# Optimization experiments

Measured on AMD Instinct MI355X. Metric: run time of the kernel, lower is better.

The kernel has to match this reference:

```python
import jax, jax.numpy as jnp
import numpy as np

DIM = 1024
NEXP = 8
TOPK = 2
B, S = 2, 2048
HID = 4 * DIM

# ---- BitLinear (kyegomez/BitNet, 1.58-bit) helpers ----

def rmsnorm(x):
    # SimpleRMSNorm: x / rms(x), no learned scale
    return x * jax.lax.rsqrt(jnp.mean(x * x, axis=-1, keepdims=True) + 1e-6)

def act_quant(x):
    # per-token int8 absmax quant
    scale = 127.0 / jnp.clip(jnp.max(jnp.abs(x), axis=-1, keepdims=True), 1e-5, None)
    return jnp.clip(jnp.round(x * scale), -128, 127) / scale

def weight_quant(w):
    # ternary weight quant with per-tensor mean-abs scale
    scale = 1.0 / jnp.clip(jnp.mean(jnp.abs(w)), 1e-5, None)
    return jnp.clip(jnp.round(w * scale), -1, 1) / scale

def ste(a, q):
    # straight-through estimator: forward q, backward identity on a
    return a + jax.lax.stop_gradient(q - a)

def bit_input(x):
    xn = rmsnorm(x)
    return ste(xn, act_quant(xn))

def bit_weight(w):
    return ste(w, weight_quant(w))


def setup_inputs() -> dict:
    key = jax.random.key(0)
    ks = jax.random.split(key, 6)
    x = jax.random.normal(ks[0], (B, S, DIM), dtype=jnp.float32)
    eps = jax.random.normal(ks[1], (B, S, NEXP), dtype=jnp.float32)
    w_route = jax.random.normal(ks[2], (NEXP, DIM), dtype=jnp.float32) * 0.02
    w_noise = jax.random.normal(ks[3], (NEXP, DIM), dtype=jnp.float32) * 0.02
    w1 = jax.random.normal(ks[4], (NEXP, HID, DIM), dtype=jnp.float32) * 0.02
    w2 = jax.random.normal(ks[5], (NEXP, DIM, HID), dtype=jnp.float32) * 0.02
    return {"x": x, "eps": eps, "w_route": w_route, "w_noise": w_noise, "w1": w1, "w2": w2}


def reference(x, eps, w_route, w_noise, w1, w2):
    Bb, Ss, D = x.shape
    # router: both BitLinears share the same rmsnorm+quant of x (no bias)
    xq = bit_input(x)                                  # [B,S,D]
    logits = xq @ bit_weight(w_route).T                # [B,S,E]
    noise_logits = xq @ bit_weight(w_noise).T          # [B,S,E]
    noisy = logits + eps * jax.nn.softplus(noise_logits)
    _, topi = jax.lax.top_k(noisy, TOPK)               # indices [B,S,K]
    sel = jnp.any(jax.nn.one_hot(topi, NEXP, dtype=jnp.bool_), axis=-2)  # [B,S,E]
    sparse = jnp.where(sel, noisy, -jnp.inf)
    gates = jax.nn.softmax(sparse, axis=-1)            # zeros at unselected experts

    T = Bb * Ss
    xf = xq.reshape(T, D)                              # expert layer-1 input quant == router's
    gf = gates.reshape(T, NEXP)
    w1q = jax.vmap(bit_weight)(w1)                     # [E,H,D]
    w2q = jax.vmap(bit_weight)(w2)                     # [E,D,H]
    h = jax.nn.relu(jnp.einsum('td,ehd->teh', xf, w1q))
    hq = bit_input(h)                                  # per-(token,expert) quant
    y = jnp.einsum('teh,edh->ted', hq, w2q)            # expert outputs
    # gated combine; gates are exactly 0 for unselected experts -> identical to masked scatter-add
    out = jnp.einsum('ted,te->td', y, gf)
    return out.reshape(Bb, Ss, D)
```

## Files before the change

### kernel.cpp

```cpp
#include <hip/hip_runtime.h>
#include <hip/hip_bf16.h>

#define DIMD 1024
#define NEXP 8
#define NTOK 4096
#define HIDN 4096
#define CAP  4096
#define EXPSTRIDE 4194304L

typedef __bf16 bf16;
typedef bf16  bf16x8 __attribute__((ext_vector_type(8)));
typedef bf16  bf16x4 __attribute__((ext_vector_type(4)));
typedef float f32x4  __attribute__((ext_vector_type(4)));

__device__ __forceinline__ void gload16(const void* g, void* l) {
  __builtin_amdgcn_global_load_lds(
      (const __attribute__((address_space(1))) unsigned int*)g,
      (__attribute__((address_space(3))) unsigned int*)l, 16, 0, 0);
}

#define VMCNT8 asm volatile("s_waitcnt vmcnt(8)" ::: "memory")
#define VMCNT0 asm volatile("s_waitcnt vmcnt(0)" ::: "memory")
#define BAR    __builtin_amdgcn_s_barrier()

__global__ void k_wsum(const float* __restrict__ w1, const float* __restrict__ w2,
                       float* __restrict__ partials) {
  const int slot = blockIdx.y;
  const int b = blockIdx.x;
  const int tid = threadIdx.x;
  const float* src = (slot < 8) ? (w1 + (long)slot * EXPSTRIDE)
                                : (w2 + (long)(slot - 8) * EXPSTRIDE);
  const f32x4* p = (const f32x4*)src;
  float s = 0.f;
  #pragma unroll
  for (int j = 0; j < 32; ++j) {
    f32x4 v = p[(long)b * 8192 + j * 256 + tid];
    s += fabsf(v.x) + fabsf(v.y) + fabsf(v.z) + fabsf(v.w);
  }
  #pragma unroll
  for (int o = 1; o < 64; o <<= 1) s += __shfl_xor(s, o, 64);
  __shared__ float red[4];
  if ((tid & 63) == 0) red[tid >> 6] = s;
  __syncthreads();
  if (tid == 0) partials[slot * 128 + b] = red[0] + red[1] + red[2] + red[3];
}

__global__ void k_finalize(const float* __restrict__ partials,
                           const float* __restrict__ wr, const float* __restrict__ wn,
                           float* __restrict__ wmean,
                           bf16* __restrict__ wrq, bf16* __restrict__ wnq) {
  const int tid = threadIdx.x;
  if (tid < 16) {
    float s = 0.f;
    for (int j = 0; j < 128; ++j) s += partials[tid * 128 + j];
    wmean[tid] = fmaxf(s * (1.0f / 4194304.0f), 1e-5f);
  }
  float sr = 0.f, sn = 0.f;
  #pragma unroll
  for (int j = 0; j < 32; ++j) {
    sr += fabsf(wr[j * 256 + tid]);
    sn += fabsf(wn[j * 256 + tid]);
  }
  #pragma unroll
  for (int o = 1; o < 64; o <<= 1) {
    sr += __shfl_xor(sr, o, 64);
    sn += __shfl_xor(sn, o, 64);
  }
  __shared__ float red[8];
  if ((tid & 63) == 0) { red[tid >> 6] = sr; red[4 + (tid >> 6)] = sn; }
  __syncthreads();
  if (tid == 0) {
    wmean[16] = fmaxf((red[0] + red[1] + red[2] + red[3]) * (1.0f / 8192.0f), 1e-5f);
    wmean[17] = fmaxf((red[4] + red[5] + red[6] + red[7]) * (1.0f / 8192.0f), 1e-5f);
  }
  __syncthreads();
  const float ir = 1.0f / wmean[16];
  const float in = 1.0f / wmean[17];
  for (int j = 0; j < 32; ++j) {
    int i = j * 256 + tid;
    wrq[i] = (bf16)fminf(fmaxf(rintf(wr[i] * ir), -1.f), 1.f);
    wnq[i] = (bf16)fminf(fmaxf(rintf(wn[i] * in), -1.f), 1.f);
  }
}

__global__ void k_wquant(const float* __restrict__ w1, const float* __restrict__ w2,
                         const float* __restrict__ wmean,
                         bf16* __restrict__ w1q, bf16* __restrict__ w2q) {
  const int tid = threadIdx.x;
  const int which = blockIdx.x >> 14;
  const long lg = (long)(blockIdx.x & 16383) * 256 + tid;
  const int e = (int)(lg >> 19);
  const float inv = 1.0f / wmean[(which ? 8 : 0) + e];
  const float* src = which ? w2 : w1;
  bf16* dst = which ? w2q : w1q;
  const f32x4* p = (const f32x4*)src + lg * 2;
  f32x4 v0 = p[0], v1 = p[1];
  bf16x8 q;
  q[0] = (bf16)fminf(fmaxf(rintf(v0.x * inv), -1.f), 1.f);
  q[1] = (bf16)fminf(fmaxf(rintf(v0.y * inv), -1.f), 1.f);
  q[2] = (bf16)fminf(fmaxf(rintf(v0.z * inv), -1.f), 1.f);
  q[3] = (bf16)fminf(fmaxf(rintf(v0.w * inv), -1.f), 1.f);
  q[4] = (bf16)fminf(fmaxf(rintf(v1.x * inv), -1.f), 1.f);
  q[5] = (bf16)fminf(fmaxf(rintf(v1.y * inv), -1.f), 1.f);
  q[6] = (bf16)fminf(fmaxf(rintf(v1.z * inv), -1.f), 1.f);
  q[7] = (bf16)fminf(fmaxf(rintf(v1.w * inv), -1.f), 1.f);
  *(bf16x8*)(dst + lg * 8) = q;
}

__global__ void k_xquant(const float* __restrict__ x, bf16* __restrict__ xq,
                         float* __restrict__ sx) {
  const int t = blockIdx.x, tid = threadIdx.x;
  f32x4 v = ((const f32x4*)(x + (long)t * DIMD))[tid];
  float ss = v.x * v.x + v.y * v.y + v.z * v.z + v.w * v.w;
  float am = fmaxf(fmaxf(fabsf(v.x), fabsf(v.y)), fmaxf(fabsf(v.z), fabsf(v.w)));
  #pragma unroll
  for (int o = 1; o < 64; o <<= 1) {
    ss += __shfl_xor(ss, o, 64);
    am = fmaxf(am, __shfl_xor(am, o, 64));
  }
  __shared__ float red[8];
  if ((tid & 63) == 0) { red[tid >> 6] = ss; red[4 + (tid >> 6)] = am; }
  __syncthreads();
  ss = red[0] + red[1] + red[2] + red[3];
  am = fmaxf(fmaxf(red[4], red[5]), fmaxf(red[6], red[7]));
  const float r = 1.0f / sqrtf(ss * (1.0f / DIMD) + 1e-6f);
  const float amn = fmaxf(am * r, 1e-5f);
  const float s = 127.0f / amn;
  bf16x4 q;
  q[0] = (bf16)fminf(fmaxf(rintf((v.x * r) * s), -128.f), 127.f);
  q[1] = (bf16)fminf(fmaxf(rintf((v.y * r) * s), -128.f), 127.f);
  q[2] = (bf16)fminf(fmaxf(rintf((v.z * r) * s), -128.f), 127.f);
  q[3] = (bf16)fminf(fmaxf(rintf((v.w * r) * s), -128.f), 127.f);
  *(bf16x4*)(xq + (long)t * DIMD + tid * 4) = q;
  if (tid == 0) sx[t] = amn * (1.0f / 127.0f);
}

__global__ void k_router(const bf16* __restrict__ xq, const float* __restrict__ sx,
                         const bf16* __restrict__ wrq, const bf16* __restrict__ wnq,
                         const float* __restrict__ eps, const float* __restrict__ wmean,
                         int* __restrict__ cnt, int* __restrict__ idx,
                         float* __restrict__ gate) {
  __shared__ float xf[DIMD];
  __shared__ float dots[16];
  const int t = blockIdx.x, tid = threadIdx.x;
  const bf16* xr = xq + (long)t * DIMD;
  #pragma unroll
  for (int j = 0; j < 4; ++j) xf[tid * 4 + j] = (float)xr[tid * 4 + j];
  __syncthreads();
  const int grp = tid >> 4, l16 = tid & 15;
  const bf16* wv = (grp < 8) ? (wrq + grp * DIMD) : (wnq + (grp - 8) * DIMD);
  float s = 0.f;
  #pragma unroll
  for (int j = 0; j < 64; ++j) s += xf[l16 + j * 16] * (float)wv[l16 + j * 16];
  s += __shfl_xor(s, 1, 64); s += __shfl_xor(s, 2, 64);
  s += __shfl_xor(s, 4, 64); s += __shfl_xor(s, 8, 64);
  if (l16 == 0) dots[grp] = s;
  __syncthreads();
  if (tid == 0) {
    const float st = sx[t];
    const float fr = st * wmean[16], fn = st * wmean[17];
    float ny[8];
    #pragma unroll
    for (int e = 0; e < 8; ++e) {
      const float nl = dots[8 + e] * fn;
      const float sp = fmaxf(nl, 0.f) + log1pf(expf(-fabsf(nl)));
      ny[e] = dots[e] * fr + eps[t * 8 + e] * sp;
    }
    int i1 = 0;
    #pragma unroll
    for (int e = 1; e < 8; ++e) if (ny[e] > ny[i1]) i1 = e;
    int i2 = (i1 == 0) ? 1 : 0;
    #pragma unroll
    for (int e = 0; e < 8; ++e) if (e != i1 && ny[e] > ny[i2]) i2 = e;
    const float ex = expf(ny[i2] - ny[i1]);
    const float g1 = 1.0f / (1.0f + ex);
    const float g2 = ex * g1;
    int p1 = atomicAdd(&cnt[i1], 1);
    idx[i1 * CAP + p1] = t; gate[i1 * CAP + p1] = g1;
    int p2 = atomicAdd(&cnt[i2], 1);
    idx[i2 * CAP + p2] = t; gate[i2 * CAP + p2] = g2;
  }
}

__global__ void k_offsets(const int* __restrict__ cnt, int* __restrict__ offs) {
  if (threadIdx.x == 0) {
    int a = 0;
    for (int e = 0; e < NEXP; ++e) { offs[e] = a; a += cnt[e]; }
    offs[8] = a;
  }
}

template <int KD, int LOGNT, bool L1>
__global__ __launch_bounds__(256, 2) void k_gemm(
    const bf16* __restrict__ Abase, const bf16* __restrict__ Wq,
    const int* __restrict__ cnt, const int* __restrict__ offs,
    const int* __restrict__ idx, const float* __restrict__ gate,
    const float* __restrict__ srow, const float* __restrict__ wmean,
    float* __restrict__ Out) {
  const int bid = blockIdx.x;
  const int xcd = bid & 7;
  const int s = bid >> 3;
  const int pl = s >> 5;
  const int mt = s & 31;
  const int pidx = pl * 8 + xcd;
  const int e = pidx >> LOGNT;
  const int nt = pidx & ((1 << LOGNT) - 1);

  const int c = cnt[e];
  if (mt * 128 >= c) return;
  const int oe = offs[e];
  __shared__ __align__(16) char lds[66048];
  char* lA0 = lds;
  char* lB0 = lds + 16384;
  char* lA1 = lds + 32768;
  char* lB1 = lds + 49152;
  int* tokL = (int*)(lds + 65536);
  const int tid = threadIdx.x, w = tid >> 6, lam = tid & 63;
  if (tid < 128) {
    int i = mt * 128 + tid;
    tokL[tid] = idx[e * CAP + (i < c ? i : c - 1)];
  }
  __syncthreads();

  const bf16* aP[4];
  const bf16* bP[4];
  #pragma unroll
  for (int i = 0; i < 4; ++i) {
    const int lrow = w * 32 + i * 8 + (lam >> 3);
    const int schunk = (lam & 7) ^ (lrow & 7);
    long arow;
    if (L1) arow = (long)tokL[lrow];
    else { int ii = mt * 128 + lrow; arow = (long)oe + (ii < c ? ii : c - 1); }
    aP[i] = Abase + arow * KD + schunk * 8;
    bP[i] = Wq + (long)e * EXPSTRIDE + (long)(nt * 128 + lrow) * KD + schunk * 8;
  }
  const int lbase = (w * 32) * 128 + lam * 16;

  auto STAGE = [&](int kb, char* dA, char* dB) {
    #pragma unroll
    for (int i = 0; i < 4; ++i) {
      gload16(aP[i] + kb * 64, dA + lbase + i * 1024);
      gload16(bP[i] + kb * 64, dB + lbase + i * 1024);
    }
  };

  const int wr = w >> 1, wc = w & 1;
  int offA[4][2], offB[4][2];
  #pragma unroll
  for (int m = 0; m < 4; ++m) {
    const int ra = wr * 64 + m * 16 + (lam & 15);
    const int rb = wc * 64 + m * 16 + (lam & 15);
    #pragma unroll
    for (int ks = 0; ks < 2; ++ks) {
      const int ch = ks * 4 + (lam >> 4);
      offA[m][ks] = ra * 128 + ((ch ^ (ra & 7)) << 4);
      offB[m][ks] = rb * 128 + ((ch ^ (rb & 7)) << 4);
    }
  }
  f32x4 acc[4][4];
  #pragma unroll
  for (int m = 0; m < 4; ++m)
    #pragma unroll
    for (int n = 0; n < 4; ++n) acc[m][n] = (f32x4){0.f, 0.f, 0.f, 0.f};

  auto COMPUTE = [&](const char* cA, const char* cB) {
    #pragma unroll
    for (int ks = 0; ks < 2; ++ks) {
      bf16x8 af[4], bfr[4];
      #pragma unroll
      for (int m = 0; m < 4; ++m) af[m] = *(const bf16x8*)(cA + offA[m][ks]);
      #pragma unroll
      for (int n = 0; n < 4; ++n) bfr[n] = *(const bf16x8*)(cB + offB[n][ks]);
      #pragma unroll
      for (int m = 0; m < 4; ++m)
        #pragma unroll
        for (int n = 0; n < 4; ++n)
          acc[m][n] = __builtin_amdgcn_mfma_f32_16x16x32_bf16(af[m], bfr[n], acc[m][n], 0, 0, 0);
    }
  };

  constexpr int KT = KD / 64;
  STAGE(0, lA0, lB0);
  for (int kb = 0; kb < KT; kb += 2) {
    STAGE(kb + 1, lA1, lB1);
    VMCNT8;
    BAR;
    COMPUTE(lA0, lB0);
    BAR;
    if (kb + 2 < KT) { STAGE(kb + 2, lA0, lB0); VMCNT8; } else { VMCNT0; }
    BAR;
    COMPUTE(lA1, lB1);
    BAR;
  }

  const float wm = wmean[(L1 ? 0 : 8) + e];
  #pragma unroll
  for (int m = 0; m < 4; ++m) {
    #pragma unroll
    for (int r = 0; r < 4; ++r) {
      const int rl = wr * 64 + m * 16 + ((lam >> 4) << 2) + r;
      const int i = mt * 128 + rl;
      if (i < c) {
        if (L1) {
          const float fac = srow[tokL[rl]] * wm;
          float* hp = Out + (long)(oe + i) * HIDN + nt * 128 + wc * 64 + (lam & 15);
          #pragma unroll
          for (int n = 0; n < 4; ++n) hp[n * 16] = fmaxf(acc[m][n][r] * fac, 0.f);
        } else {
          const float fac = srow[oe + i] * wm * gate[e * CAP + i];
          float* op = Out + (long)tokL[rl] * DIMD + nt * 128 + wc * 64 + (lam & 15);
          #pragma unroll
          for (int n = 0; n < 4; ++n) atomicAdd(op + n * 16, acc[m][n][r] * fac);
        }
      }
    }
  }
}

__global__ void k_hquant(const float* __restrict__ h, bf16* __restrict__ hq,
                         float* __restrict__ sh, const int* __restrict__ offs) {
  const int row = blockIdx.x;
  if (row >= offs[8]) return;
  const int tid = threadIdx.x;
  const f32x4* hr = (const f32x4*)(h + (long)row * HIDN);
  f32x4 v[4];
  float ss = 0.f, am = 0.f;
  #pragma unroll
  for (int j = 0; j < 4; ++j) {
    v[j] = hr[tid + j * 256];
    ss += v[j].x * v[j].x + v[j].y * v[j].y + v[j].z * v[j].z + v[j].w * v[j].w;
    am = fmaxf(am, fmaxf(fmaxf(fabsf(v[j].x), fabsf(v[j].y)),
                         fmaxf(fabsf(v[j].z), fabsf(v[j].w))));
  }
  #pragma unroll
  for (int o = 1; o < 64; o <<= 1) {
    ss += __shfl_xor(ss, o, 64);
    am = fmaxf(am, __shfl_xor(am, o, 64));
  }
  __shared__ float red[8];
  if ((tid & 63) == 0) { red[tid >> 6] = ss; red[4 + (tid >> 6)] = am; }
  __syncthreads();
  ss = red[0] + red[1] + red[2] + red[3];
  am = fmaxf(fmaxf(red[4], red[5]), fmaxf(red[6], red[7]));
  const float r = 1.0f / sqrtf(ss * (1.0f / HIDN) + 1e-6f);
  const float amn = fmaxf(am * r, 1e-5f);
  const float s = 127.0f / amn;
  bf16* dst = hq + (long)row * HIDN;
  #pragma unroll
  for (int j = 0; j < 4; ++j) {
    bf16x4 q;
    q[0] = (bf16)fminf(fmaxf(rintf((v[j].x * r) * s), -128.f), 127.f);
    q[1] = (bf16)fminf(fmaxf(rintf((v[j].y * r) * s), -128.f), 127.f);
    q[2] = (bf16)fminf(fmaxf(rintf((v[j].z * r) * s), -128.f), 127.f);
    q[3] = (bf16)fminf(fmaxf(rintf((v[j].w * r) * s), -128.f), 127.f);
    *(bf16x4*)(dst + (tid + j * 256) * 4) = q;
  }
  if (tid == 0) sh[row] = amn * (1.0f / 127.0f);
}

extern "C" void kernel_launch(void* const* d_in, const int* in_sizes, int n_in,
                              void* d_out, int out_size, void* d_ws, size_t ws_size,
                              hipStream_t stream) {
  const float* x   = (const float*)d_in[0];
  const float* eps = (const float*)d_in[1];
  const float* wr  = (const float*)d_in[2];
  const float* wn  = (const float*)d_in[3];
  const float* w1  = (const float*)d_in[4];
  const float* w2  = (const float*)d_in[5];
  float* out = (float*)d_out;
  (void)in_sizes; (void)n_in; (void)ws_size;

  char* ws = (char*)d_ws;
  size_t off = 0;
  auto alloc = [&](size_t bytes) -> void* {
    void* p = ws + off;
    off = (off + bytes + 255) & ~(size_t)255;
    return p;
  };
  bf16*  w1q      = (bf16*)alloc(67108864);
  bf16*  w2q      = (bf16*)alloc(67108864);
  bf16*  wrq      = (bf16*)alloc(16384);
  bf16*  wnq      = (bf16*)alloc(16384);
  bf16*  xq       = (bf16*)alloc(8388608);
  float* sx       = (float*)alloc(16384);
  float* sh       = (float*)alloc(32768);
  int*   idxb     = (int*)alloc(131072);
  float* gateb    = (float*)alloc(131072);
  int*   cntb     = (int*)alloc(64);
  int*   offsb    = (int*)alloc(64);
  float* partials = (float*)alloc(8192);
  float* wmean    = (float*)alloc(128);
  float* h        = (float*)alloc(134217728);
  bf16*  hq       = (bf16*)alloc(67108864);

  hipMemsetAsync(out, 0, (size_t)out_size * sizeof(float), stream);
  hipMemsetAsync(cntb, 0, 64, stream);

  k_wsum<<<dim3(128, 16), 256, 0, stream>>>(w1, w2, partials);
  k_finalize<<<1, 256, 0, stream>>>(partials, wr, wn, wmean, wrq, wnq);
  k_wquant<<<32768, 256, 0, stream>>>(w1, w2, wmean, w1q, w2q);
  k_xquant<<<NTOK, 256, 0, stream>>>(x, xq, sx);
  k_router<<<NTOK, 256, 0, stream>>>(xq, sx, wrq, wnq, eps, wmean, cntb, idxb, gateb);
  k_offsets<<<1, 64, 0, stream>>>(cntb, offsb);
  k_gemm<1024, 5, true><<<8192, 256, 0, stream>>>(
      xq, w1q, cntb, offsb, idxb, gateb, sx, wmean, h);
  k_hquant<<<8192, 256, 0, stream>>>(h, hq, sh, offsb);
  k_gemm<4096, 3, false><<<2048, 256, 0, stream>>>(
      hq, w2q, cntb, offsb, idxb, gateb, sh, wmean, out);
}
```

Before: 762.0 us.

## Switch expert GEMMs from bf16 to int8 MFMA with int8 quantized storage

Stores quantized weights, activations and hidden states as int8 instead of bf16, and replaces the bf16 16x16x32 MFMA with the i32 16x16x64 int8 MFMA. LDS staging, swizzle and load pointers are reworked for 64-byte int8 K tiles, which halves LDS use and lets launch bounds request 4 blocks per CU. Values are already integers within int8 range, so results should stay exact with int32 accumulation. This halves memory traffic for the quantized tensors and doubles MFMA throughput per instruction.

After: 661.3 us. 1.15x faster.

```diff
diff --git a/kernel.cpp b/kernel.cpp
--- a/kernel.cpp
+++ b/kernel.cpp
@@ -10,8 +10,11 @@
 
 typedef __bf16 bf16;
 typedef bf16  bf16x8 __attribute__((ext_vector_type(8)));
-typedef bf16  bf16x4 __attribute__((ext_vector_type(4)));
 typedef float f32x4  __attribute__((ext_vector_type(4)));
+typedef int   i32x4  __attribute__((ext_vector_type(4)));
+typedef signed char i8x8 __attribute__((ext_vector_type(8)));
+typedef signed char i8x4 __attribute__((ext_vector_type(4)));
+typedef signed char i8;
 
 __device__ __forceinline__ void gload16(const void* g, void* l) {
   __builtin_amdgcn_global_load_lds(
@@ -19,9 +22,9 @@
       (__attribute__((address_space(3))) unsigned int*)l, 16, 0, 0);
 }
 
-#define VMCNT8 asm volatile("s_waitcnt vmcnt(8)" ::: "memory")
+#define VMCNT4 asm volatile("s_waitcnt vmcnt(4)" ::: "memory")
 #define VMCNT0 asm volatile("s_waitcnt vmcnt(0)" ::: "memory")
-#define BAR    __builtin_amdgcn_s_barrier()
+#define BAR    asm volatile("s_barrier" ::: "memory")
 
 __global__ void k_wsum(const float* __restrict__ w1, const float* __restrict__ w2,
                        float* __restrict__ partials) {
@@ -85,29 +88,29 @@
 
 __global__ void k_wquant(const float* __restrict__ w1, const float* __restrict__ w2,
                          const float* __restrict__ wmean,
-                         bf16* __restrict__ w1q, bf16* __restrict__ w2q) {
+                         i8* __restrict__ w1q, i8* __restrict__ w2q) {
   const int tid = threadIdx.x;
   const int which = blockIdx.x >> 14;
   const long lg = (long)(blockIdx.x & 16383) * 256 + tid;
   const int e = (int)(lg >> 19);
   const float inv = 1.0f / wmean[(which ? 8 : 0) + e];
   const float* src = which ? w2 : w1;
-  bf16* dst = which ? w2q : w1q;
+  i8* dst = which ? w2q : w1q;
   const f32x4* p = (const f32x4*)src + lg * 2;
   f32x4 v0 = p[0], v1 = p[1];
-  bf16x8 q;
-  q[0] = (bf16)fminf(fmaxf(rintf(v0.x * inv), -1.f), 1.f);
-  q[1] = (bf16)fminf(fmaxf(rintf(v0.y * inv), -1.f), 1.f);
-  q[2] = (bf16)fminf(fmaxf(rintf(v0.z * inv), -1.f), 1.f);
-  q[3] = (bf16)fminf(fmaxf(rintf(v0.w * inv), -1.f), 1.f);
-  q[4] = (bf16)fminf(fmaxf(rintf(v1.x * inv), -1.f), 1.f);
-  q[5] = (bf16)fminf(fmaxf(rintf(v1.y * inv), -1.f), 1.f);
-  q[6] = (bf16)fminf(fmaxf(rintf(v1.z * inv), -1.f), 1.f);
-  q[7] = (bf16)fminf(fmaxf(rintf(v1.w * inv), -1.f), 1.f);
-  *(bf16x8*)(dst + lg * 8) = q;
-}
-
-__global__ void k_xquant(const float* __restrict__ x, bf16* __restrict__ xq,
+  i8x8 q;
+  q[0] = (i8)fminf(fmaxf(rintf(v0.x * inv), -1.f), 1.f);
+  q[1] = (i8)fminf(fmaxf(rintf(v0.y * inv), -1.f), 1.f);
+  q[2] = (i8)fminf(fmaxf(rintf(v0.z * inv), -1.f), 1.f);
+  q[3] = (i8)fminf(fmaxf(rintf(v0.w * inv), -1.f), 1.f);
+  q[4] = (i8)fminf(fmaxf(rintf(v1.x * inv), -1.f), 1.f);
+  q[5] = (i8)fminf(fmaxf(rintf(v1.y * inv), -1.f), 1.f);
+  q[6] = (i8)fminf(fmaxf(rintf(v1.z * inv), -1.f), 1.f);
+  q[7] = (i8)fminf(fmaxf(rintf(v1.w * inv), -1.f), 1.f);
+  *(i8x8*)(dst + lg * 8) = q;
+}
+
+__global__ void k_xquant(const float* __restrict__ x, i8* __restrict__ xq,
                          float* __restrict__ sx) {
   const int t = blockIdx.x, tid = threadIdx.x;
   f32x4 v = ((const f32x4*)(x + (long)t * DIMD))[tid];
@@ -126,16 +129,16 @@
   const float r = 1.0f / sqrtf(ss * (1.0f / DIMD) + 1e-6f);
   const float amn = fmaxf(am * r, 1e-5f);
   const float s = 127.0f / amn;
-  bf16x4 q;
-  q[0] = (bf16)fminf(fmaxf(rintf((v.x * r) * s), -128.f), 127.f);
-  q[1] = (bf16)fminf(fmaxf(rintf((v.y * r) * s), -128.f), 127.f);
-  q[2] = (bf16)fminf(fmaxf(rintf((v.z * r) * s), -128.f), 127.f);
-  q[3] = (bf16)fminf(fmaxf(rintf((v.w * r) * s), -128.f), 127.f);
-  *(bf16x4*)(xq + (long)t * DIMD + tid * 4) = q;
+  i8x4 q;
+  q[0] = (i8)fminf(fmaxf(rintf((v.x * r) * s), -128.f), 127.f);
+  q[1] = (i8)fminf(fmaxf(rintf((v.y * r) * s), -128.f), 127.f);
+  q[2] = (i8)fminf(fmaxf(rintf((v.z * r) * s), -128.f), 127.f);
+  q[3] = (i8)fminf(fmaxf(rintf((v.w * r) * s), -128.f), 127.f);
+  *(i8x4*)(xq + (long)t * DIMD + tid * 4) = q;
   if (tid == 0) sx[t] = amn * (1.0f / 127.0f);
 }
 
-__global__ void k_router(const bf16* __restrict__ xq, const float* __restrict__ sx,
+__global__ void k_router(const i8* __restrict__ xq, const float* __restrict__ sx,
                          const bf16* __restrict__ wrq, const bf16* __restrict__ wnq,
                          const float* __restrict__ eps, const float* __restrict__ wmean,
                          int* __restrict__ cnt, int* __restrict__ idx,
@@ -143,7 +146,7 @@
   __shared__ float xf[DIMD];
   __shared__ float dots[16];
   const int t = blockIdx.x, tid = threadIdx.x;
-  const bf16* xr = xq + (long)t * DIMD;
+  const i8* xr = xq + (long)t * DIMD;
   #pragma unroll
   for (int j = 0; j < 4; ++j) xf[tid * 4 + j] = (float)xr[tid * 4 + j];
   __syncthreads();
@@ -191,8 +194,8 @@
 }
 
 template <int KD, int LOGNT, bool L1>
-__global__ __launch_bounds__(256, 2) void k_gemm(
-    const bf16* __restrict__ Abase, const bf16* __restrict__ Wq,
+__global__ __launch_bounds__(256, 4) void k_gemm(
+    const i8* __restrict__ Abase, const i8* __restrict__ Wq,
     const int* __restrict__ cnt, const int* __restrict__ offs,
     const int* __restrict__ idx, const float* __restrict__ gate,
     const float* __restrict__ srow, const float* __restrict__ wmean,
@@ -209,12 +212,12 @@
   const int c = cnt[e];
   if (mt * 128 >= c) return;
   const int oe = offs[e];
-  __shared__ __align__(16) char lds[66048];
+  __shared__ __align__(16) char lds[33280];
   char* lA0 = lds;
-  char* lB0 = lds + 16384;
-  char* lA1 = lds + 32768;
-  char* lB1 = lds + 49152;
-  int* tokL = (int*)(lds + 65536);
+  char* lB0 = lds + 8192;
+  char* lA1 = lds + 16384;
+  char* lB1 = lds + 24576;
+  int* tokL = (int*)(lds + 32768);
   const int tid = threadIdx.x, w = tid >> 6, lam = tid & 63;
   if (tid < 128) {
     int i = mt * 128 + tid;
@@ -222,72 +225,66 @@
   }
   __syncthreads();
 
-  const bf16* aP[4];
-  const bf16* bP[4];
-  #pragma unroll
-  for (int i = 0; i < 4; ++i) {
-    const int lrow = w * 32 + i * 8 + (lam >> 3);
-    const int schunk = (lam & 7) ^ (lrow & 7);
+  const i8* aS[2];
+  const i8* bS[2];
+  #pragma unroll
+  for (int i = 0; i < 2; ++i) {
+    const int cid = w * 64 + lam + 256 * i;
+    const int r = cid >> 2, q = cid & 3;
+    const int cg = q ^ ((r >> 1) & 3);
     long arow;
-    if (L1) arow = (long)tokL[lrow];
-    else { int ii = mt * 128 + lrow; arow = (long)oe + (ii < c ? ii : c - 1); }
-    aP[i] = Abase + arow * KD + schunk * 8;
-    bP[i] = Wq + (long)e * EXPSTRIDE + (long)(nt * 128 + lrow) * KD + schunk * 8;
-  }
-  const int lbase = (w * 32) * 128 + lam * 16;
+    if (L1) arow = (long)tokL[r];
+    else { int ii = mt * 128 + r; arow = (long)oe + (ii < c ? ii : c - 1); }
+    aS[i] = Abase + arow * KD + cg * 16;
+    bS[i] = Wq + (long)e * EXPSTRIDE + (long)(nt * 128 + r) * KD + cg * 16;
+  }
+  const int dbase = (w * 64 + lam) * 16;
 
   auto STAGE = [&](int kb, char* dA, char* dB) {
     #pragma unroll
-    for (int i = 0; i < 4; ++i) {
-      gload16(aP[i] + kb * 64, dA + lbase + i * 1024);
-      gload16(bP[i] + kb * 64, dB + lbase + i * 1024);
-    }
+    for (int i = 0; i < 2; ++i) gload16(aS[i] + kb * 64, dA + dbase + i * 4096);
+    #pragma unroll
+    for (int i = 0; i < 2; ++i) gload16(bS[i] + kb * 64, dB + dbase + i * 4096);
   };
 
   const int wr = w >> 1, wc = w & 1;
-  int offA[4][2], offB[4][2];
+  int offA[4], offB[4];
+  const int cc = lam >> 4;
   #pragma unroll
   for (int m = 0; m < 4; ++m) {
     const int ra = wr * 64 + m * 16 + (lam & 15);
     const int rb = wc * 64 + m * 16 + (lam & 15);
-    #pragma unroll
-    for (int ks = 0; ks < 2; ++ks) {
-      const int ch = ks * 4 + (lam >> 4);
-      offA[m][ks] = ra * 128 + ((ch ^ (ra & 7)) << 4);
-      offB[m][ks] = rb * 128 + ((ch ^ (rb & 7)) << 4);
-    }
-  }
-  f32x4 acc[4][4];
+    offA[m] = ra * 64 + ((cc ^ ((ra >> 1) & 3)) << 4);
+    offB[m] = rb * 64 + ((cc ^ ((rb >> 1) & 3)) << 4);
+  }
+  i32x4 acc[4][4];
   #pragma unroll
   for (int m = 0; m < 4; ++m)
     #pragma unroll
-    for (int n = 0; n < 4; ++n) acc[m][n] = (f32x4){0.f, 0.f, 0.f, 0.f};
+    for (int n = 0; n < 4; ++n) acc[m][n] = (i32x4){0, 0, 0, 0};
 
   auto COMPUTE = [&](const char* cA, const char* cB) {
-    #pragma unroll
-    for (int ks = 0; ks < 2; ++ks) {
-      bf16x8 af[4], bfr[4];
+    i32x4 af[4], bfr[4];
+    #pragma unroll
+    for (int m = 0; m < 4; ++m) af[m] = *(const i32x4*)(cA + offA[m]);
+    #pragma unroll
+    for (int n = 0; n < 4; ++n) bfr[n] = *(const i32x4*)(cB + offB[n]);
+    #pragma unroll
+    for (int m = 0; m < 4; ++m)
       #pragma unroll
-      for (int m = 0; m < 4; ++m) af[m] = *(const bf16x8*)(cA + offA[m][ks]);
-      #pragma unroll
-      for (int n = 0; n < 4; ++n) bfr[n] = *(const bf16x8*)(cB + offB[n][ks]);
-      #pragma unroll
-      for (int m = 0; m < 4; ++m)
-        #pragma unroll
-        for (int n = 0; n < 4; ++n)
-          acc[m][n] = __builtin_amdgcn_mfma_f32_16x16x32_bf16(af[m], bfr[n], acc[m][n], 0, 0, 0);
-    }
+      for (int n = 0; n < 4; ++n)
+        acc[m][n] = __builtin_amdgcn_mfma_i32_16x16x64_i8(af[m], bfr[n], acc[m][n], 0, 0, 0);
   };
 
   constexpr int KT = KD / 64;
   STAGE(0, lA0, lB0);
   for (int kb = 0; kb < KT; kb += 2) {
     STAGE(kb + 1, lA1, lB1);
-    VMCNT8;
+    VMCNT4;
     BAR;
     COMPUTE(lA0, lB0);
     BAR;
-    if (kb + 2 < KT) { STAGE(kb + 2, lA0, lB0); VMCNT8; } else { VMCNT0; }
+    if (kb + 2 < KT) { STAGE(kb + 2, lA0, lB0); VMCNT4; } else { VMCNT0; }
     BAR;
     COMPUTE(lA1, lB1);
     BAR;
@@ -305,19 +302,19 @@
           const float fac = srow[tokL[rl]] * wm;
           float* hp = Out + (long)(oe + i) * HIDN + nt * 128 + wc * 64 + (lam & 15);
           #pragma unroll
-          for (int n = 0; n < 4; ++n) hp[n * 16] = fmaxf(acc[m][n][r] * fac, 0.f);
+          for (int n = 0; n < 4; ++n) hp[n * 16] = fmaxf((float)acc[m][n][r] * fac, 0.f);
         } else {
           const float fac = srow[oe + i] * wm * gate[e * CAP + i];
           float* op = Out + (long)tokL[rl] * DIMD + nt * 128 + wc * 64 + (lam & 15);
           #pragma unroll
-          for (int n = 0; n < 4; ++n) atomicAdd(op + n * 16, acc[m][n][r] * fac);
+          for (int n = 0; n < 4; ++n) atomicAdd(op + n * 16, (float)acc[m][n][r] * fac);
         }
       }
     }
   }
 }
 
-__global__ void k_hquant(const float* __restrict__ h, bf16* __restrict__ hq,
+__global__ void k_hquant(const float* __restrict__ h, i8* __restrict__ hq,
                          float* __restrict__ sh, const int* __restrict__ offs) {
   const int row = blockIdx.x;
   if (row >= offs[8]) return;
@@ -345,15 +342,15 @@
   const float r = 1.0f / sqrtf(ss * (1.0f / HIDN) + 1e-6f);
   const float amn = fmaxf(am * r, 1e-5f);
   const float s = 127.0f / amn;
-  bf16* dst = hq + (long)row * HIDN;
+  i8* dst = hq + (long)row * HIDN;
   #pragma unroll
   for (int j = 0; j < 4; ++j) {
-    bf16x4 q;
-    q[0] = (bf16)fminf(fmaxf(rintf((v[j].x * r) * s), -128.f), 127.f);
-    q[1] = (bf16)fminf(fmaxf(rintf((v[j].y * r) * s), -128.f), 127.f);
-    q[2] = (bf16)fminf(fmaxf(rintf((v[j].z * r) * s), -128.f), 127.f);
-    q[3] = (bf16)fminf(fmaxf(rintf((v[j].w * r) * s), -128.f), 127.f);
-    *(bf16x4*)(dst + (tid + j * 256) * 4) = q;
+    i8x4 q;
+    q[0] = (i8)fminf(fmaxf(rintf((v[j].x * r) * s), -128.f), 127.f);
+    q[1] = (i8)fminf(fmaxf(rintf((v[j].y * r) * s), -128.f), 127.f);
+    q[2] = (i8)fminf(fmaxf(rintf((v[j].z * r) * s), -128.f), 127.f);
+    q[3] = (i8)fminf(fmaxf(rintf((v[j].w * r) * s), -128.f), 127.f);
+    *(i8x4*)(dst + (tid + j * 256) * 4) = q;
   }
   if (tid == 0) sh[row] = amn * (1.0f / 127.0f);
 }
@@ -377,11 +374,11 @@
     off = (off + bytes + 255) & ~(size_t)255;
     return p;
   };
-  bf16*  w1q      = (bf16*)alloc(67108864);
-  bf16*  w2q      = (bf16*)alloc(67108864);
+  i8*    w1q      = (i8*)alloc(33554432);
+  i8*    w2q      = (i8*)alloc(33554432);
   bf16*  wrq      = (bf16*)alloc(16384);
   bf16*  wnq      = (bf16*)alloc(16384);
-  bf16*  xq       = (bf16*)alloc(8388608);
+  i8*    xq       = (i8*)alloc(4194304);
   float* sx       = (float*)alloc(16384);
   float* sh       = (float*)alloc(32768);
   int*   idxb     = (int*)alloc(131072);
@@ -391,10 +388,10 @@
   float* partials = (float*)alloc(8192);
   float* wmean    = (float*)alloc(128);
   float* h        = (float*)alloc(134217728);
-  bf16*  hq       = (bf16*)alloc(67108864);
-
-  hipMemsetAsync(out, 0, (size_t)out_size * sizeof(float), stream);
-  hipMemsetAsync(cntb, 0, 64, stream);
+  i8*    hq       = (i8*)alloc(33554432);
+
+  (void)hipMemsetAsync(out, 0, (size_t)out_size * sizeof(float), stream);
+  (void)hipMemsetAsync(cntb, 0, 64, stream);
 
   k_wsum<<<dim3(128, 16), 256, 0, stream>>>(w1, w2, partials);
   k_finalize<<<1, 256, 0, stream>>>(partials, wr, wn, wmean, wrq, wnq);
```
